# Performance work log

Hardware: AMD Instinct MI355X
Metric: run time of the kernel (lower is better)

Reference implementation:

```python
import jax, jax.numpy as jnp
import numpy as np

N_NODES = 100000
N_EDGES = 1600000
N_GRAPHS = 64
C_IN = 64
HID = 64
N_CLASSES = 10
EPS = 1e-5


def setup_inputs() -> dict:
    key = jax.random.key(0)
    ks = jax.random.split(key, 12)
    x = jax.random.normal(ks[0], (N_NODES, C_IN), dtype=jnp.float32)
    edge_index = jax.random.randint(ks[1], (2, N_EDGES), 0, N_NODES, dtype=jnp.int64)
    batch = jnp.sort(jax.random.randint(ks[2], (N_NODES,), 0, N_GRAPHS, dtype=jnp.int64))

    def lin(k, fan_in, fan_out):
        lim = 1.0 / np.sqrt(fan_in)
        kw, kb = jax.random.split(k)
        W = jax.random.uniform(kw, (fan_in, fan_out), minval=-lim, maxval=lim, dtype=jnp.float32)
        b = jax.random.uniform(kb, (fan_out,), minval=-lim, maxval=lim, dtype=jnp.float32)
        return W, b

    W1, b1 = lin(ks[3], 2 * C_IN, HID)
    W2, b2 = lin(ks[4], 2 * HID, HID)
    W3, b3 = lin(ks[5], 2 * HID, HID)
    Wo, bo = lin(ks[6], HID, N_CLASSES)
    g1 = jnp.ones((HID,), jnp.float32); be1 = jnp.zeros((HID,), jnp.float32)
    g2 = jnp.ones((HID,), jnp.float32); be2 = jnp.zeros((HID,), jnp.float32)
    g3 = jnp.ones((HID,), jnp.float32); be3 = jnp.zeros((HID,), jnp.float32)
    return {"x": x, "edge_index": edge_index, "batch": batch,
            "W1": W1, "b1": b1, "W2": W2, "b2": b2, "W3": W3, "b3": b3,
            "g1": g1, "be1": be1, "g2": g2, "be2": be2, "g3": g3, "be3": be3,
            "Wo": Wo, "bo": bo}


def edge_conv(x, src, dst, W, b):
    # PyG EdgeConv: message = mlp(cat([x_i, x_j - x_i])), aggr = max over incoming edges
    xi = x[dst]                       # target node feats [E, C]
    xj = x[src]                       # source node feats [E, C]
    m = jax.nn.relu(jnp.concatenate([xi, xj - xi], axis=-1) @ W + b)  # [E, H]
    out = jax.ops.segment_max(m, dst, num_segments=N_NODES)
    return jnp.where(jnp.isfinite(out), out, 0.0)  # nodes with no edges -> 0


def batch_norm(x, g, b):
    # training-mode BatchNorm1d over node axis, biased variance
    mu = jnp.mean(x, axis=0)
    var = jnp.mean(jnp.square(x - mu), axis=0)
    return (x - mu) * jax.lax.rsqrt(var + EPS) * g + b


def reference(x, edge_index, batch, W1, b1, W2, b2, W3, b3,
              g1, be1, g2, be2, g3, be3, Wo, bo):
    src, dst = edge_index[0], edge_index[1]
    h = edge_conv(x, src, dst, W1, b1)
    h = jax.nn.relu(batch_norm(h, g1, be1))
    h = edge_conv(h, src, dst, W2, b2)
    h = jax.nn.relu(batch_norm(h, g2, be2))
    h = edge_conv(h, src, dst, W3, b3)
    h = batch_norm(h, g3, be3)
    # global mean pool over graphs
    sums = jax.ops.segment_sum(h, batch, num_segments=N_GRAPHS)        # [G, H]
    cnts = jax.ops.segment_sum(jnp.ones((h.shape[0],), h.dtype), batch, num_segments=N_GRAPHS)
    pooled = sums / jnp.maximum(cnts, 1.0)[:, None]
    logits = pooled @ Wo + bo
    return jax.nn.softmax(logits, axis=1)
```

## Files before the change

### kernel.cpp

```cpp
#include <hip/hip_runtime.h>
#include <hip/hip_bf16.h>
#include <math.h>

#define N_NODES 100000
#define N_EDGES 1600000
#define N_GRAPHS 64
#define EPS 1e-5f
#define NBUCK 391
#define BSTRIDE 6144
#define BSCAT_GRID 196
#define SEG_NBLK 3125
#define GEMM_TILES 1563

typedef unsigned int u32;
typedef __attribute__((ext_vector_type(8))) short short8;
typedef __attribute__((ext_vector_type(4))) float f32x4;

static __device__ __forceinline__ ushort f2bf(float f) {
  u32 x = __float_as_uint(f);
  u32 r = (x + 0x7fffu + ((x >> 16) & 1u)) >> 16;
  return (ushort)r;
}
static __device__ __forceinline__ float bflo(u32 w) { return __uint_as_float(w << 16); }
static __device__ __forceinline__ float bfhi(u32 w) { return __uint_as_float(w & 0xffff0000u); }
static __device__ __forceinline__ void decode8(uint4 w, float* f) {
  f[0] = bflo(w.x); f[1] = bfhi(w.x); f[2] = bflo(w.y); f[3] = bfhi(w.y);
  f[4] = bflo(w.z); f[5] = bfhi(w.z); f[6] = bflo(w.w); f[7] = bfhi(w.w);
}

__global__ __launch_bounds__(256) void bscat_setup_k(
    const int* __restrict__ src, const int* __restrict__ dst,
    u32* __restrict__ bcur, u32* __restrict__ pairs,
    const float* __restrict__ W1, const float* __restrict__ W2,
    const float* __restrict__ W3, uint4* __restrict__ Wb,
    const int* __restrict__ batch, u32* __restrict__ bounds,
    u32* __restrict__ zbase) {
  __shared__ u32 cnt[NBUCK];
  __shared__ u32 base[NBUCK];
  int bid = blockIdx.x, t = threadIdx.x;
  if (bid < BSCAT_GRID) {
    for (int i = t; i < NBUCK; i += 256) cnt[i] = 0;
    __syncthreads();
    u32 pk[32], bk[32];
    int be = bid * 8192;
#pragma unroll
    for (int k = 0; k < 32; ++k) {
      int e = be + k * 256 + t;
      if (e < N_EDGES) {
        u32 d = (u32)dst[e], s = (u32)src[e];
        u32 b = d >> 8;
        pk[k] = ((d & 255u) << 24) | s;
        bk[k] = b;
        atomicAdd(&cnt[b], 1u);
      } else bk[k] = 0xFFFFFFFFu;
    }
    __syncthreads();
    for (int i = t; i < NBUCK; i += 256) {
      u32 c = cnt[i];
      base[i] = c ? (i * BSTRIDE + atomicAdd(&bcur[i], c)) : 0u;
      cnt[i] = 0;
    }
    __syncthreads();
#pragma unroll
    for (int k = 0; k < 32; ++k) {
      if (bk[k] != 0xFFFFFFFFu) {
        u32 p = base[bk[k]] + atomicAdd(&cnt[bk[k]], 1u);
        pairs[p] = pk[k];
      }
    }
  } else if (bid < BSCAT_GRID + 12) {
    int g = (bid - BSCAT_GRID) * 256 + t;
    if (g >= 3072) return;
    int layer = g >> 10, rem = g & 1023;
    int kh = rem >> 9, ct = (rem >> 6) & 7, l = rem & 63;
    const float* W = (layer == 0) ? W1 : (layer == 1) ? W2 : W3;
    int c = ct * 16 + (l & 15);
    u32 w[4];
#pragma unroll
    for (int jj = 0; jj < 4; ++jj) {
      int k0 = kh * 32 + (l >> 4) * 8 + 2 * jj;
      float v0, v1;
      if (c < 64) {
        v0 = W[k0 * 64 + c] - W[(64 + k0) * 64 + c];
        v1 = W[(k0 + 1) * 64 + c] - W[(65 + k0) * 64 + c];
      } else {
        v0 = W[(64 + k0) * 64 + (c - 64)];
        v1 = W[(65 + k0) * 64 + (c - 64)];
      }
      w[jj] = (u32)f2bf(v0) | ((u32)f2bf(v1) << 16);
    }
    Wb[g] = make_uint4(w[0], w[1], w[2], w[3]);
  } else if (bid == BSCAT_GRID + 12) {
    if (t > 64) return;
    int lo = 0, hi = N_NODES;
    while (lo < hi) {
      int mid = (lo + hi) >> 1;
      if (batch[mid] < t) lo = mid + 1; else hi = mid;
    }
    bounds[t] = (u32)lo;
  } else {
    for (int i = t; i < 16448; i += 256) zbase[i] = 0u;
  }
}

static __device__ __forceinline__ void fscat2_body(
    int b, u32* SH, const u32* __restrict__ bcur, const u32* __restrict__ pairs,
    u32* __restrict__ esrc, u32* __restrict__ offs_g, u32* __restrict__ cnt_g) {
  u32* lcnt = SH; u32* lexc = SH + 256; u32* lcur = SH + 512;
  int t = threadIdx.x;
  u32 s0 = b * BSTRIDE, e0 = s0 + bcur[b];
  lcnt[t] = 0;
  __syncthreads();
  for (u32 p = s0 + t; p < e0; p += 256) atomicAdd(&lcnt[pairs[p] >> 24], 1u);
  __syncthreads();
  u32 v = lcnt[t];
  lexc[t] = v;
  __syncthreads();
  for (int d = 1; d < 256; d <<= 1) {
    u32 a = (t >= d) ? lexc[t - d] : 0u;
    __syncthreads();
    lexc[t] += a;
    __syncthreads();
  }
  u32 excl = lexc[t] - v;
  int node = (b << 8) + t;
  if (node < N_NODES) { offs_g[node] = s0 + excl; cnt_g[node] = v; }
  lcur[t] = 0;
  lexc[t] = excl;
  __syncthreads();
  for (u32 p = s0 + t; p < e0; p += 256) {
    u32 pk = pairs[p];
    u32 dl = pk >> 24;
    u32 l = atomicAdd(&lcur[dl], 1u);
    esrc[s0 + lexc[dl] + l] = pk & 0x00FFFFFFu;
  }
}

static __device__ __forceinline__ void gemm_body(
    int tile, u32* Xl,
    const void* __restrict__ xin, int xbf16, const uint4* __restrict__ Wb,
    const float* ab, const float* __restrict__ bias,
    ushort* __restrict__ ub, ushort* __restrict__ vb) {
  int t = threadIdx.x;
  int l = t & 63, wv = t >> 6;
  short8 bs[2][8];
#pragma unroll
  for (int kh = 0; kh < 2; ++kh)
#pragma unroll
    for (int ct = 0; ct < 8; ++ct) {
      uint4 tmp = Wb[(kh * 8 + ct) * 64 + l];
      __builtin_memcpy(&bs[kh][ct], &tmp, 16);
    }
  int srow = t >> 2, scol = (t & 3) * 16;
  int rb = tile * 64;
  int gr = rb + srow;
  u32 xb[8];
  if (gr < N_NODES) {
    if (xbf16) {
      const uint4* xp = (const uint4*)((const ushort*)xin + (size_t)gr * 64 + scol);
      uint4 p0 = xp[0], p1 = xp[1];
      u32 raw[8] = {p0.x, p0.y, p0.z, p0.w, p1.x, p1.y, p1.z, p1.w};
#pragma unroll
      for (int q = 0; q < 8; ++q) {
        int c = scol + 2 * q;
        float lo = fmaxf(fmaf(bflo(raw[q]), ab[c], ab[64 + c]), 0.f);
        float hi = fmaxf(fmaf(bfhi(raw[q]), ab[c + 1], ab[64 + c + 1]), 0.f);
        xb[q] = (u32)f2bf(lo) | ((u32)f2bf(hi) << 16);
      }
    } else {
      const float4* xp = (const float4*)((const float*)xin + (size_t)gr * 64 + scol);
#pragma unroll
      for (int q = 0; q < 4; ++q) {
        float4 a = xp[q];
        xb[2 * q]     = (u32)f2bf(a.x) | ((u32)f2bf(a.y) << 16);
        xb[2 * q + 1] = (u32)f2bf(a.z) | ((u32)f2bf(a.w) << 16);
      }
    }
  } else {
#pragma unroll
    for (int q = 0; q < 8; ++q) xb[q] = 0u;
  }
  int byte0 = srow * 128 + ((scol * 2) ^ ((srow & 7) << 4));
  int byte1 = srow * 128 + ((scol * 2 + 16) ^ ((srow & 7) << 4));
  *(uint4*)((char*)Xl + byte0) = make_uint4(xb[0], xb[1], xb[2], xb[3]);
  *(uint4*)((char*)Xl + byte1) = make_uint4(xb[4], xb[5], xb[6], xb[7]);
  __syncthreads();
  f32x4 acc[8];
#pragma unroll
  for (int ct = 0; ct < 8; ++ct) {
    float b0 = (ct < 4) ? bias[ct * 16 + (l & 15)] : 0.f;
    acc[ct] = (f32x4){b0, b0, b0, b0};
  }
  int arow = wv * 16 + (l & 15);
#pragma unroll
  for (int kh = 0; kh < 2; ++kh) {
    int abyte = arow * 128 + ((kh * 64 + ((l >> 4) * 16)) ^ ((arow & 7) << 4));
    short8 af = *(const short8*)((const char*)Xl + abyte);
#pragma unroll
    for (int ct = 0; ct < 8; ++ct)
      acc[ct] = __builtin_amdgcn_mfma_f32_16x16x32_bf16(af, bs[kh][ct], acc[ct], 0, 0, 0);
  }
  int rloc = rb + wv * 16 + 4 * (l >> 4);
#pragma unroll
  for (int ct = 0; ct < 4; ++ct) {
    int col = ct * 16 + (l & 15);
#pragma unroll
    for (int r = 0; r < 4; ++r) {
      int row = rloc + r;
      if (row < N_NODES) ub[(size_t)row * 64 + col] = f2bf(acc[ct][r]);
    }
  }
#pragma unroll
  for (int ct = 4; ct < 8; ++ct) {
    int col = ct * 16 + (l & 15) - 64;
#pragma unroll
    for (int r = 0; r < 4; ++r) {
      int row = rloc + r;
      if (row < N_NODES) vb[(size_t)row * 64 + col] = f2bf(acc[ct][r]);
    }
  }
}

__global__ __launch_bounds__(256) void fused_fg_k(
    const u32* __restrict__ bcur, const u32* __restrict__ pairs,
    u32* __restrict__ esrc, u32* __restrict__ offs_g, u32* __restrict__ cnt_g,
    const float* __restrict__ x, const uint4* __restrict__ Wb,
    const float* __restrict__ bias, ushort* __restrict__ ub, ushort* __restrict__ vb) {
  __shared__ u32 SH[2048];
  int bid = blockIdx.x;
  if (bid < NBUCK) fscat2_body(bid, SH, bcur, pairs, esrc, offs_g, cnt_g);
  else gemm_body(bid - NBUCK, SH, x, 0, Wb, nullptr, bias, ub, vb);
}

__global__ __launch_bounds__(256) void gemm_k(
    const ushort* __restrict__ xin, const uint4* __restrict__ Wb,
    const float* __restrict__ bnacc, const float* __restrict__ g,
    const float* __restrict__ be, const float* __restrict__ bias,
    ushort* __restrict__ ub, ushort* __restrict__ vb) {
  __shared__ u32 Xl[2048];
  __shared__ float ab_sh[128];
  int t = threadIdx.x;
  if (t < 64) {
    float s1 = 0.f, s2 = 0.f;
    for (int s = 0; s < 32; ++s) {
      s1 += bnacc[s * 128 + t];
      s2 += bnacc[s * 128 + 64 + t];
    }
    float mu = s1 / (float)N_NODES;
    float var = s2 / (float)N_NODES - mu * mu;
    float al = g[t] / sqrtf(var + EPS);
    ab_sh[t] = al;
    ab_sh[64 + t] = be[t] - mu * al;
  }
  __syncthreads();
  gemm_body(blockIdx.x, Xl, xin, 1, Wb, ab_sh, bias, ub, vb);
}

__global__ __launch_bounds__(256) void segmax_k(
    const ushort* __restrict__ v, const u32* __restrict__ offs,
    const u32* __restrict__ cnt, const u32* __restrict__ esrc,
    const ushort* __restrict__ ub, ushort* __restrict__ hb,
    float* __restrict__ bnacc) {
  int t = threadIdx.x;
  int lane = t & 63;
  int op = lane & 7;
  int sub = lane >> 3;
  int wv = t >> 6;
  int node = blockIdx.x * 32 + wv * 8 + sub;
  const uint4* v4 = (const uint4*)v;
  const uint4* u4 = (const uint4*)ub;
  uint4* h4 = (uint4*)hb;
  u32 off = offs[node], deg = cnt[node];
  const u32* ep = esrc + off;
  float m[8];
#pragma unroll
  for (int j = 0; j < 8; ++j) m[j] = -INFINITY;
  u32 i = 0;
  for (; i + 4 <= deg; i += 4) {
    u32 sA = ep[i], sB = ep[i + 1], sC = ep[i + 2], sD = ep[i + 3];
    uint4 wA = v4[(size_t)sA * 8 + op];
    uint4 wB = v4[(size_t)sB * 8 + op];
    uint4 wC = v4[(size_t)sC * 8 + op];
    uint4 wD = v4[(size_t)sD * 8 + op];
    float fA[8], fB[8], fC[8], fD[8];
    decode8(wA, fA); decode8(wB, fB); decode8(wC, fC); decode8(wD, fD);
#pragma unroll
    for (int j = 0; j < 8; ++j)
      m[j] = fmaxf(fmaxf(m[j], fmaxf(fA[j], fB[j])), fmaxf(fC[j], fD[j]));
  }
  for (; i < deg; ++i) {
    uint4 w = v4[(size_t)ep[i] * 8 + op];
    float f[8]; decode8(w, f);
#pragma unroll
    for (int j = 0; j < 8; ++j) m[j] = fmaxf(m[j], f[j]);
  }
  uint4 uu = u4[(size_t)node * 8 + op];
  float uf[8]; decode8(uu, uf);
  float h[8];
#pragma unroll
  for (int j = 0; j < 8; ++j) h[j] = fmaxf(uf[j] + m[j], 0.f);
  uint4 hw;
  hw.x = (u32)f2bf(h[0]) | ((u32)f2bf(h[1]) << 16);
  hw.y = (u32)f2bf(h[2]) | ((u32)f2bf(h[3]) << 16);
  hw.z = (u32)f2bf(h[4]) | ((u32)f2bf(h[5]) << 16);
  hw.w = (u32)f2bf(h[6]) | ((u32)f2bf(h[7]) << 16);
  h4[(size_t)node * 8 + op] = hw;
  __shared__ float red[2048];
#pragma unroll
  for (int j = 0; j < 8; ++j) red[t * 8 + j] = h[j];
  __syncthreads();
  float o1 = 0.f, o2 = 0.f;
  if (t < 64) {
    int cop = t >> 3, cj = t & 7;
    for (int q = 0; q < 32; ++q) o1 += red[(q * 8 + cop) * 8 + cj];
  }
  __syncthreads();
#pragma unroll
  for (int j = 0; j < 8; ++j) red[t * 8 + j] = h[j] * h[j];
  __syncthreads();
  if (t < 64) {
    int cop = t >> 3, cj = t & 7;
    for (int q = 0; q < 32; ++q) o2 += red[(q * 8 + cop) * 8 + cj];
    int slice = blockIdx.x & 31;
    atomicAdd(&bnacc[slice * 128 + t], o1);
    atomicAdd(&bnacc[slice * 128 + 64 + t], o2);
  }
}

__global__ __launch_bounds__(256) void pool_part_k(
    const ushort* __restrict__ h3, const u32* __restrict__ bounds,
    float* __restrict__ sums) {
  int g = blockIdx.y;
  u32 s = bounds[g], e = bounds[g + 1];
  int t = threadIdx.x;
  int op = t & 7;
  int slot = blockIdx.x * 32 + (t >> 3);
  int nsl = gridDim.x * 32;
  const uint4* h4 = (const uint4*)h3;
  float acc[8];
#pragma unroll
  for (int j = 0; j < 8; ++j) acc[j] = 0.f;
  for (u32 n = s + slot; n < e; n += nsl) {
    uint4 w = h4[(size_t)n * 8 + op];
    float f[8]; decode8(w, f);
#pragma unroll
    for (int j = 0; j < 8; ++j) acc[j] += f[j];
  }
  __shared__ float red[2048];
#pragma unroll
  for (int j = 0; j < 8; ++j) red[t * 8 + j] = acc[j];
  __syncthreads();
  if (t < 64) {
    int cop = t >> 3, cj = t & 7;
    float o = 0.f;
    for (int q = 0; q < 32; ++q) o += red[(q * 8 + cop) * 8 + cj];
    atomicAdd(&sums[g * 64 + t], o);
  }
}

__global__ void head_k(const float* __restrict__ sums, const u32* __restrict__ bounds,
                       const float* __restrict__ bnacc3, const float* __restrict__ g3,
                       const float* __restrict__ be3, const float* __restrict__ Wo,
                       const float* __restrict__ bo, float* __restrict__ out) {
  __shared__ float ab3[128];
  int t = threadIdx.x;
  if (t < 64) {
    float s1 = 0.f, s2 = 0.f;
    for (int sl = 0; sl < 32; ++sl) {
      s1 += bnacc3[sl * 128 + t];
      s2 += bnacc3[sl * 128 + 64 + t];
    }
    float mu = s1 / (float)N_NODES;
    float var = s2 / (float)N_NODES - mu * mu;
    float al = g3[t] / sqrtf(var + EPS);
    ab3[t] = al;
    ab3[64 + t] = be3[t] - mu * al;
  }
  __syncthreads();
  if (t >= N_GRAPHS) return;
  u32 cntn = bounds[t + 1] - bounds[t];
  float inv = (cntn > 0) ? 1.f / (float)cntn : 0.f;
  float lg[10];
#pragma unroll
  for (int j = 0; j < 10; ++j) lg[j] = bo[j];
  for (int c = 0; c < 64; ++c) {
    float p = (cntn > 0) ? (sums[t * 64 + c] * inv * ab3[c] + ab3[64 + c]) : 0.f;
#pragma unroll
    for (int j = 0; j < 10; ++j) lg[j] = fmaf(p, Wo[c * 10 + j], lg[j]);
  }
  float mx = lg[0];
#pragma unroll
  for (int j = 1; j < 10; ++j) mx = fmaxf(mx, lg[j]);
  float ssum = 0.f, ex[10];
#pragma unroll
  for (int j = 0; j < 10; ++j) { ex[j] = expf(lg[j] - mx); ssum += ex[j]; }
#pragma unroll
  for (int j = 0; j < 10; ++j) out[t * 10 + j] = ex[j] / ssum;
}

extern "C" void kernel_launch(void* const* d_in, const int* in_sizes, int n_in,
                              void* d_out, int out_size, void* d_ws, size_t ws_size,
                              hipStream_t stream) {
  const float* x    = (const float*)d_in[0];
  const int*   ei   = (const int*)d_in[1];
  const int*   batch= (const int*)d_in[2];
  const float* W1 = (const float*)d_in[3];  const float* b1 = (const float*)d_in[4];
  const float* W2 = (const float*)d_in[5];  const float* b2 = (const float*)d_in[6];
  const float* W3 = (const float*)d_in[7];  const float* b3 = (const float*)d_in[8];
  const float* g1 = (const float*)d_in[9];  const float* be1= (const float*)d_in[10];
  const float* g2 = (const float*)d_in[11]; const float* be2= (const float*)d_in[12];
  const float* g3 = (const float*)d_in[13]; const float* be3= (const float*)d_in[14];
  const float* Wo = (const float*)d_in[15]; const float* bo = (const float*)d_in[16];
  float* out = (float*)d_out;

  char* p = (char*)d_ws;
  auto alloc = [&](size_t bytes) { void* r = (void*)p; p += (bytes + 255) & ~(size_t)255; return r; };
  uint4* Wb     = (uint4*)alloc(3072 * sizeof(uint4));
  u32*   bounds = (u32*)alloc(65 * sizeof(u32));
  u32*   bcur   = (u32*)alloc(NBUCK * sizeof(u32));
  u32*   cnt    = (u32*)alloc((size_t)N_NODES * sizeof(u32));
  u32*   offs   = (u32*)alloc((size_t)N_NODES * sizeof(u32));
  float* sums   = (float*)alloc(4096 * sizeof(float));
  float* bnacc  = (float*)alloc(12288 * sizeof(float));
  u32*   esrc   = (u32*)alloc((size_t)NBUCK * BSTRIDE * sizeof(u32));
  u32*   pairs  = (u32*)alloc((size_t)NBUCK * BSTRIDE * sizeof(u32));
  ushort* ub    = (ushort*)alloc((size_t)N_NODES * 64 * sizeof(ushort));
  ushort* vb    = (ushort*)alloc((size_t)N_NODES * 64 * sizeof(ushort));
  ushort* hb    = (ushort*)alloc((size_t)N_NODES * 64 * sizeof(ushort));

  const int* src = ei;
  const int* dst = ei + N_EDGES;

  hipMemsetAsync(bcur, 0, NBUCK * sizeof(u32), stream);
  bscat_setup_k<<<BSCAT_GRID + 14, 256, 0, stream>>>(src, dst, bcur, pairs,
                                                     W1, W2, W3, Wb, batch, bounds,
                                                     (u32*)sums);

  fused_fg_k<<<NBUCK + GEMM_TILES, 256, 0, stream>>>(bcur, pairs, esrc, offs, cnt,
                                                     x, Wb, b1, ub, vb);
  segmax_k<<<SEG_NBLK, 256, 0, stream>>>(vb, offs, cnt, esrc, ub, hb, bnacc);

  gemm_k<<<GEMM_TILES, 256, 0, stream>>>(hb, Wb + 1024, bnacc, g1, be1, b2, ub, vb);
  segmax_k<<<SEG_NBLK, 256, 0, stream>>>(vb, offs, cnt, esrc, ub, hb, bnacc + 4096);

  gemm_k<<<GEMM_TILES, 256, 0, stream>>>(hb, Wb + 2048, bnacc + 4096, g2, be2, b3, ub, vb);
  segmax_k<<<SEG_NBLK, 256, 0, stream>>>(vb, offs, cnt, esrc, ub, hb, bnacc + 8192);

  pool_part_k<<<dim3(16, N_GRAPHS), 256, 0, stream>>>(hb, bounds, sums);
  head_k<<<1, 64, 0, stream>>>(sums, bounds, bnacc + 8192, g3, be3, Wo, bo, out);
}
```

Baseline: 205.5 us.

## Fuse global mean-pool partial sums into last segmax and drop pool kernel

The final segment-max pass is templated so its LAST instance skips writing h3 to memory. Instead it finds each node's graph by binary search over the graph bounds and does a block-level reduction of per-graph sums with atomics into the pool buffer. This removes the separate pool kernel launch and its full re-read of h3. The hipMemsetAsync on the bucket counters is also replaced by a tiny zero kernel, and the zeroing range in setup shrinks. The cost is extra shared-memory reductions and atomics in the last segmax, plus a per-element atomic path for blocks that span more than two graphs.

Result: no change. 202.9 us (-1.3%).

```diff
diff --git a/kernel.cpp b/kernel.cpp
--- a/kernel.cpp
+++ b/kernel.cpp
@@ -26,6 +26,11 @@
 static __device__ __forceinline__ void decode8(uint4 w, float* f) {
   f[0] = bflo(w.x); f[1] = bfhi(w.x); f[2] = bflo(w.y); f[3] = bfhi(w.y);
   f[4] = bflo(w.z); f[5] = bfhi(w.z); f[6] = bflo(w.w); f[7] = bfhi(w.w);
+}
+
+__global__ void zero_k(u32* __restrict__ p, int n) {
+  int i = blockIdx.x * 256 + threadIdx.x;
+  if (i < n) p[i] = 0u;
 }
 
 __global__ __launch_bounds__(256) void bscat_setup_k(
@@ -99,7 +104,7 @@
     }
     bounds[t] = (u32)lo;
   } else {
-    for (int i = t; i < 16448; i += 256) zbase[i] = 0u;
+    for (int i = t; i < 16384; i += 256) zbase[i] = 0u;
   }
 }
 
@@ -256,12 +261,22 @@
   gemm_body(blockIdx.x, Xl, xin, 1, Wb, ab_sh, bias, ub, vb);
 }
 
+template <int LAST>
 __global__ __launch_bounds__(256) void segmax_k(
     const ushort* __restrict__ v, const u32* __restrict__ offs,
     const u32* __restrict__ cnt, const u32* __restrict__ esrc,
     const ushort* __restrict__ ub, ushort* __restrict__ hb,
-    float* __restrict__ bnacc) {
+    float* __restrict__ bnacc, const u32* __restrict__ bounds,
+    float* __restrict__ sums) {
+  __shared__ float red[2048];
+  __shared__ u32 bsh[65];
+  __shared__ int gmin_sh, mflag;
   int t = threadIdx.x;
+  if (LAST) {
+    if (t < 65) bsh[t] = bounds[t];
+    if (t == 0) mflag = 0;
+    __syncthreads();
+  }
   int lane = t & 63;
   int op = lane & 7;
   int sub = lane >> 3;
@@ -269,7 +284,6 @@
   int node = blockIdx.x * 32 + wv * 8 + sub;
   const uint4* v4 = (const uint4*)v;
   const uint4* u4 = (const uint4*)ub;
-  uint4* h4 = (uint4*)hb;
   u32 off = offs[node], deg = cnt[node];
   const u32* ep = esrc + off;
   float m[8];
@@ -299,19 +313,29 @@
   float h[8];
 #pragma unroll
   for (int j = 0; j < 8; ++j) h[j] = fmaxf(uf[j] + m[j], 0.f);
-  uint4 hw;
-  hw.x = (u32)f2bf(h[0]) | ((u32)f2bf(h[1]) << 16);
-  hw.y = (u32)f2bf(h[2]) | ((u32)f2bf(h[3]) << 16);
-  hw.z = (u32)f2bf(h[4]) | ((u32)f2bf(h[5]) << 16);
-  hw.w = (u32)f2bf(h[6]) | ((u32)f2bf(h[7]) << 16);
-  h4[(size_t)node * 8 + op] = hw;
-  __shared__ float red[2048];
+  int g = 0;
+  if (LAST) {
+    int lo = 0, hi = N_GRAPHS - 1;
+    while (lo < hi) {
+      int mid = (lo + hi + 1) >> 1;
+      if (bsh[mid] <= (u32)node) lo = mid; else hi = mid - 1;
+    }
+    g = lo;
+    if (t == 0) gmin_sh = g;
+  } else {
+    uint4 hw;
+    hw.x = (u32)f2bf(h[0]) | ((u32)f2bf(h[1]) << 16);
+    hw.y = (u32)f2bf(h[2]) | ((u32)f2bf(h[3]) << 16);
+    hw.z = (u32)f2bf(h[4]) | ((u32)f2bf(h[5]) << 16);
+    hw.w = (u32)f2bf(h[6]) | ((u32)f2bf(h[7]) << 16);
+    ((uint4*)hb)[(size_t)node * 8 + op] = hw;
+  }
 #pragma unroll
   for (int j = 0; j < 8; ++j) red[t * 8 + j] = h[j];
   __syncthreads();
   float o1 = 0.f, o2 = 0.f;
+  int cop = t >> 3, cj = t & 7;
   if (t < 64) {
-    int cop = t >> 3, cj = t & 7;
     for (int q = 0; q < 32; ++q) o1 += red[(q * 8 + cop) * 8 + cj];
   }
   __syncthreads();
@@ -319,42 +343,39 @@
   for (int j = 0; j < 8; ++j) red[t * 8 + j] = h[j] * h[j];
   __syncthreads();
   if (t < 64) {
-    int cop = t >> 3, cj = t & 7;
     for (int q = 0; q < 32; ++q) o2 += red[(q * 8 + cop) * 8 + cj];
     int slice = blockIdx.x & 31;
     atomicAdd(&bnacc[slice * 128 + t], o1);
     atomicAdd(&bnacc[slice * 128 + 64 + t], o2);
   }
-}
-
-__global__ __launch_bounds__(256) void pool_part_k(
-    const ushort* __restrict__ h3, const u32* __restrict__ bounds,
-    float* __restrict__ sums) {
-  int g = blockIdx.y;
-  u32 s = bounds[g], e = bounds[g + 1];
-  int t = threadIdx.x;
-  int op = t & 7;
-  int slot = blockIdx.x * 32 + (t >> 3);
-  int nsl = gridDim.x * 32;
-  const uint4* h4 = (const uint4*)h3;
-  float acc[8];
-#pragma unroll
-  for (int j = 0; j < 8; ++j) acc[j] = 0.f;
-  for (u32 n = s + slot; n < e; n += nsl) {
-    uint4 w = h4[(size_t)n * 8 + op];
-    float f[8]; decode8(w, f);
-#pragma unroll
-    for (int j = 0; j < 8; ++j) acc[j] += f[j];
-  }
-  __shared__ float red[2048];
-#pragma unroll
-  for (int j = 0; j < 8; ++j) red[t * 8 + j] = acc[j];
-  __syncthreads();
-  if (t < 64) {
-    int cop = t >> 3, cj = t & 7;
-    float o = 0.f;
-    for (int q = 0; q < 32; ++q) o += red[(q * 8 + cop) * 8 + cj];
-    atomicAdd(&sums[g * 64 + t], o);
+  if (LAST) {
+    __syncthreads();
+    int gmin = gmin_sh;
+    int slot = g - gmin;
+#pragma unroll
+    for (int j = 0; j < 8; ++j) red[t * 8 + j] = (slot == 0) ? h[j] : 0.f;
+    if (slot != 0) mflag = 1;
+    __syncthreads();
+    if (t < 64) {
+      float o = 0.f;
+      for (int q = 0; q < 32; ++q) o += red[(q * 8 + cop) * 8 + cj];
+      atomicAdd(&sums[gmin * 64 + t], o);
+    }
+    if (mflag) {
+      __syncthreads();
+#pragma unroll
+      for (int j = 0; j < 8; ++j) red[t * 8 + j] = (slot == 1) ? h[j] : 0.f;
+      __syncthreads();
+      if (t < 64) {
+        float o = 0.f;
+        for (int q = 0; q < 32; ++q) o += red[(q * 8 + cop) * 8 + cj];
+        atomicAdd(&sums[(gmin + 1) * 64 + t], o);
+      }
+      if (slot >= 2) {
+#pragma unroll
+        for (int j = 0; j < 8; ++j) atomicAdd(&sums[g * 64 + op * 8 + j], h[j]);
+      }
+    }
   }
 }
 
@@ -431,21 +452,23 @@
   const int* src = ei;
   const int* dst = ei + N_EDGES;
 
-  hipMemsetAsync(bcur, 0, NBUCK * sizeof(u32), stream);
+  zero_k<<<2, 256, 0, stream>>>(bcur, NBUCK);
   bscat_setup_k<<<BSCAT_GRID + 14, 256, 0, stream>>>(src, dst, bcur, pairs,
                                                      W1, W2, W3, Wb, batch, bounds,
                                                      (u32*)sums);
 
   fused_fg_k<<<NBUCK + GEMM_TILES, 256, 0, stream>>>(bcur, pairs, esrc, offs, cnt,
                                                      x, Wb, b1, ub, vb);
-  segmax_k<<<SEG_NBLK, 256, 0, stream>>>(vb, offs, cnt, esrc, ub, hb, bnacc);
+  segmax_k<0><<<SEG_NBLK, 256, 0, stream>>>(vb, offs, cnt, esrc, ub, hb, bnacc,
+                                            bounds, sums);
 
   gemm_k<<<GEMM_TILES, 256, 0, stream>>>(hb, Wb + 1024, bnacc, g1, be1, b2, ub, vb);
-  segmax_k<<<SEG_NBLK, 256, 0, stream>>>(vb, offs, cnt, esrc, ub, hb, bnacc + 4096);
+  segmax_k<0><<<SEG_NBLK, 256, 0, stream>>>(vb, offs, cnt, esrc, ub, hb, bnacc + 4096,
+                                            bounds, sums);
 
   gemm_k<<<GEMM_TILES, 256, 0, stream>>>(hb, Wb + 2048, bnacc + 4096, g2, be2, b3, ub, vb);
-  segmax_k<<<SEG_NBLK, 256, 0, stream>>>(vb, offs, cnt, esrc, ub, hb, bnacc + 8192);
-
-  pool_part_k<<<dim3(16, N_GRAPHS), 256, 0, stream>>>(hb, bounds, sums);
+  segmax_k<1><<<SEG_NBLK, 256, 0, stream>>>(vb, offs, cnt, esrc, ub, hb, bnacc + 8192,
+                                            bounds, sums);
+
   head_k<<<1, 64, 0, stream>>>(sums, bounds, bnacc + 8192, g3, be3, Wo, bo, out);
 }
```
